# Optimization experiments

Measured on AMD Instinct MI355X. Metric: run time of the kernel, lower is better.

Reference implementation:

```python
import jax, jax.numpy as jnp
import numpy as np

B, S, HID = 2, 2048, 2048
H, HKV = 16, 4
D = HID // H          # 128
N_REP = H // HKV      # 4
ROPE_THETA = 1000000.0


def _rope_tables(seq_len, head_dim, theta):
    inv_freq = 1.0 / (theta ** (jnp.arange(0, head_dim, 2, dtype=jnp.float32) / head_dim))
    freqs = jnp.arange(seq_len, dtype=jnp.float32)[:, None] * inv_freq[None, :]  # [S, D/2]
    emb = jnp.concatenate([freqs, freqs], axis=-1)  # [S, D]
    return jnp.cos(emb), jnp.sin(emb)


def setup_inputs() -> dict:
    key = jax.random.key(0)
    ks = jax.random.split(key, 6)
    cos, sin = _rope_tables(S, D, ROPE_THETA)
    sc = 0.02
    return {
        "x": jax.random.normal(ks[0], (B, S, HID), jnp.float32),
        "cos": cos,
        "sin": sin,
        "Wq": jax.random.normal(ks[1], (HID, H * D), jnp.float32) * sc,
        "Wk": jax.random.normal(ks[2], (HID, HKV * D), jnp.float32) * sc,
        "Wv": jax.random.normal(ks[3], (HID, HKV * D), jnp.float32) * sc,
        "Wo": jax.random.normal(ks[4], (H * D, HID), jnp.float32) * sc,
    }


def _rotate_half(t):
    t1, t2 = jnp.split(t, 2, axis=-1)
    return jnp.concatenate([-t2, t1], axis=-1)


def reference(x, cos, sin, Wq, Wk, Wv, Wo):
    b, s, _ = x.shape
    q = (x @ Wq).reshape(b, s, H, D)    # [b,s,H,d]
    k = (x @ Wk).reshape(b, s, HKV, D)  # [b,s,Hkv,d]
    v = (x @ Wv).reshape(b, s, HKV, D)

    # RoPE (cos/sin broadcast over head axis)
    c = cos[:s, None, :]  # [s,1,d]
    sn = sin[:s, None, :]
    q = q * c + _rotate_half(q) * sn
    k = k * c + _rotate_half(k) * sn

    # GQA: repeat kv heads (interleaved, matching repeat_kv)
    k = jnp.repeat(k, N_REP, axis=2)  # [b,s,H,d]
    v = jnp.repeat(v, N_REP, axis=2)

    q = q.transpose(0, 2, 1, 3)  # [b,H,s,d]
    k = k.transpose(0, 2, 1, 3)
    v = v.transpose(0, 2, 1, 3)

    scale = 1.0 / jnp.sqrt(jnp.asarray(D, x.dtype))
    scores = jnp.einsum("bhqd,bhkd->bhqk", q, k) * scale
    causal = jnp.tril(jnp.ones((s, s), dtype=bool))
    scores = jnp.where(causal[None, None], scores, jnp.asarray(-jnp.inf, scores.dtype))
    probs = jax.nn.softmax(scores, axis=-1)
    out = jnp.einsum("bhqk,bhkd->bhqd", probs, v)
    out = out.transpose(0, 2, 1, 3).reshape(b, s, H * D)
    return out @ Wo
```

## Files before the change

### kernel.cpp

```cpp
#include <hip/hip_runtime.h>
#include <cstdint>

#define B_    2
#define S_    2048
#define HID_  2048
#define H_    16
#define HKV_  4
#define D_    128
#define SCALE_ 0.08838834764831845f
#define LOG2E_ 1.4426950408889634f
#define K1_   (SCALE_ * LOG2E_)
#define THRS_ 62.75f

typedef __bf16 bf16x8 __attribute__((ext_vector_type(8)));
typedef float  f32x4  __attribute__((ext_vector_type(4)));
using u16 = unsigned short;

static __device__ __forceinline__ u16 f2bf(float f) {
  union { float f; uint32_t u; } c; c.f = f;
  uint32_t u = c.u;
  return (u16)((u + 0x7FFFu + ((u >> 16) & 1u)) >> 16);
}
static __device__ __forceinline__ float bf2f(u16 h) {
  union { uint32_t u; float f; } c; c.u = ((uint32_t)h) << 16;
  return c.f;
}
static __device__ __forceinline__ void async16(const u16* g, u16* lds) {
  __builtin_amdgcn_global_load_lds((const __attribute__((address_space(1))) void*)g,
                                   (__attribute__((address_space(3))) void*)lds, 16, 0, 0);
}

__global__ __launch_bounds__(256) void prep_cast_weights(const float* __restrict__ x,
                                                         const float* __restrict__ Wq,
                                                         const float* __restrict__ Wk,
                                                         const float* __restrict__ Wv,
                                                         const float* __restrict__ Wo,
                                                         u16* __restrict__ xb,
                                                         u16* __restrict__ Wt,
                                                         u16* __restrict__ Wot) {
  __shared__ float tile[32][33];
  const int t = blockIdx.x;
  const int tid = threadIdx.x;
  if (t < 8192) {
    const int i = t * 256 + tid;
    float4 v = ((const float4*)x)[i];
    ushort4 o;
    o.x = f2bf(v.x); o.y = f2bf(v.y); o.z = f2bf(v.z); o.w = f2bf(v.w);
    ((ushort4*)xb)[i] = o;
    return;
  }
  const int tw = t - 8192;
  const float* W; u16* Dst; int N, lt;
  if (tw < 4096)      { W = Wq; Dst = Wt;                        N = 2048; lt = tw; }
  else if (tw < 5120) { W = Wk; Dst = Wt + (size_t)2048 * 2048;  N = 512;  lt = tw - 4096; }
  else if (tw < 6144) { W = Wv; Dst = Wt + (size_t)2560 * 2048;  N = 512;  lt = tw - 5120; }
  else                { W = Wo; Dst = Wot;                       N = 2048; lt = tw - 6144; }
  const int tx = tid & 31, ty = tid >> 5;
  const int tn = N >> 5;
  const int n0 = (lt % tn) * 32, k0 = (lt / tn) * 32;
#pragma unroll
  for (int j = 0; j < 32; j += 8)
    tile[ty + j][tx] = W[(size_t)(k0 + ty + j) * N + n0 + tx];
  __syncthreads();
#pragma unroll
  for (int j = 0; j < 32; j += 8)
    Dst[(size_t)(n0 + ty + j) * 2048 + k0 + tx] = f2bf(tile[tx][ty + j]);
}

__global__ __launch_bounds__(256) void prep_rope_vt(const u16* __restrict__ qkv,
                                                    const float* __restrict__ cosb,
                                                    const float* __restrict__ sinb,
                                                    u16* __restrict__ Qr, u16* __restrict__ Kr,
                                                    u16* __restrict__ Vt) {
  __shared__ u16 tile[32][34];
  const int NQ2 = B_ * S_ * H_ * 32;
  const int NK2 = B_ * S_ * HKV_ * 32;
  const int blk = blockIdx.x;
  const int tid = threadIdx.x;
  if (blk < 10240) {
    const int idx = blk * 256 + tid;
    if (idx < NQ2) {
      const int j = (idx & 31) * 2, rest = idx >> 5;
      const int h = rest & 15, srow = rest >> 4;
      const int s = srow & (S_ - 1);
      const u16* base = qkv + (size_t)srow * 3072 + h * 128;
      const float2 cc = *(const float2*)&cosb[s * 128 + j];
      const float2 ss = *(const float2*)&sinb[s * 128 + j];
      const ushort2 av = *(const ushort2*)&base[j];
      const ushort2 bv = *(const ushort2*)&base[j + 64];
      const float a0 = bf2f(av.x), a1 = bf2f(av.y);
      const float b0 = bf2f(bv.x), b1 = bf2f(bv.y);
      const size_t qo = (((size_t)(srow >> 11) * H_ + h) * S_ + s) * D_;
      ushort2 lo, hi;
      lo.x = f2bf(a0 * cc.x - b0 * ss.x); lo.y = f2bf(a1 * cc.y - b1 * ss.y);
      hi.x = f2bf(b0 * cc.x + a0 * ss.x); hi.y = f2bf(b1 * cc.y + a1 * ss.y);
      *(ushort2*)&Qr[qo + j]      = lo;
      *(ushort2*)&Qr[qo + j + 64] = hi;
    } else if (idx < NQ2 + NK2) {
      const int t2 = idx - NQ2;
      const int j = (t2 & 31) * 2, rest = t2 >> 5;
      const int kv = rest & 3, srow = rest >> 2;
      const int s = srow & (S_ - 1);
      const u16* base = qkv + (size_t)srow * 3072 + 2048 + kv * 128;
      const float2 cc = *(const float2*)&cosb[s * 128 + j];
      const float2 ss = *(const float2*)&sinb[s * 128 + j];
      const ushort2 av = *(const ushort2*)&base[j];
      const ushort2 bv = *(const ushort2*)&base[j + 64];
      const float a0 = bf2f(av.x), a1 = bf2f(av.y);
      const float b0 = bf2f(bv.x), b1 = bf2f(bv.y);
      const size_t ko = (((size_t)(srow >> 11) * HKV_ + kv) * S_ + s) * D_;
      ushort2 lo, hi;
      lo.x = f2bf(a0 * cc.x - b0 * ss.x); lo.y = f2bf(a1 * cc.y - b1 * ss.y);
      hi.x = f2bf(b0 * cc.x + a0 * ss.x); hi.y = f2bf(b1 * cc.y + a1 * ss.y);
      *(ushort2*)&Kr[ko + j]      = lo;
      *(ushort2*)&Kr[ko + j + 64] = hi;
    }
    return;
  }
  const int lt = blk - 10240;
  const int bx = lt & 3, by = (lt >> 2) & 63, mat = lt >> 8;
  const int b = mat >> 2, kv = mat & 3;
  const int d0 = bx * 32, s0 = by * 32;
  const int tx = tid & 31, ty = tid >> 5;
#pragma unroll
  for (int j = 0; j < 32; j += 8)
    tile[ty + j][tx] = qkv[(size_t)(b * S_ + s0 + ty + j) * 3072 + 2560 + kv * 128 + d0 + tx];
  __syncthreads();
  const int sc  = s0 + tx;
  const int t64 = sc & 63;
  const int p   = ((t64 >> 5) * 4 + ((t64 >> 2) & 3)) * 8 + ((t64 >> 4) & 1) * 4 + (t64 & 3);
  const int scp = (sc & ~63) | p;
#pragma unroll
  for (int j = 0; j < 32; j += 8)
    Vt[((size_t)mat * D_ + d0 + ty + j) * S_ + scp] = tile[tx][ty + j];
}

template<int BF16OUT>
__global__ __launch_bounds__(256, 3) void gemm_bt(const u16* __restrict__ A,
                                                  const u16* __restrict__ Bt,
                                                  void* __restrict__ Cv,
                                                  int M, int N, int K, int gx) {
  const int nwg = (int)gridDim.x;
  const int bid = (int)blockIdx.x;
  const int qq = nwg >> 3, rr = nwg & 7;
  const int xcd = bid & 7, pos = bid >> 3;
  const int wg = ((xcd < rr) ? xcd * (qq + 1) : rr * (qq + 1) + (xcd - rr) * qq) + pos;
  const int bm = (wg % gx) * 128;
  const int bn = (wg / gx) * 128;

  __shared__ __align__(16) u16 Ash[128 * 64];
  __shared__ __align__(16) u16 Bsh[128 * 64];
  const int tid = threadIdx.x;
  const int w = tid >> 6, l = tid & 63;
  const int wm = (w >> 1) * 64, wn = (w & 1) * 64;

  const f32x4 z4 = {0.f, 0.f, 0.f, 0.f};
  f32x4 acc[4][4];
#pragma unroll
  for (int i = 0; i < 4; ++i)
#pragma unroll
    for (int j = 0; j < 4; ++j) acc[i][j] = z4;

  const int srow = w * 8 + (l >> 3);
  const int schunk = l & 7;

  for (int k0 = 0; k0 < K; k0 += 64) {
#pragma unroll
    for (int i = 0; i < 4; ++i) {
      const int row = i * 32 + srow;
      const int ch = schunk ^ (row & 7);
      async16(A + (size_t)(bm + row) * K + k0 + ch * 8, &Ash[(i * 4 + w) * 512]);
      async16(Bt + (size_t)(bn + row) * K + k0 + ch * 8, &Bsh[(i * 4 + w) * 512]);
    }
    asm volatile("s_waitcnt vmcnt(0)" ::: "memory");
    __syncthreads();
#pragma unroll
    for (int kc = 0; kc < 2; ++kc) {
      bf16x8 af[4], bfr[4];
#pragma unroll
      for (int mi = 0; mi < 4; ++mi) {
        const int r = wm + mi * 16 + (l & 15);
        const int c2 = (kc * 4 + (l >> 4)) ^ (r & 7);
        af[mi] = *(const bf16x8*)&Ash[r * 64 + c2 * 8];
      }
#pragma unroll
      for (int ni = 0; ni < 4; ++ni) {
        const int r = wn + ni * 16 + (l & 15);
        const int c2 = (kc * 4 + (l >> 4)) ^ (r & 7);
        bfr[ni] = *(const bf16x8*)&Bsh[r * 64 + c2 * 8];
      }
#pragma unroll
      for (int mi = 0; mi < 4; ++mi)
#pragma unroll
        for (int ni = 0; ni < 4; ++ni)
          acc[mi][ni] = __builtin_amdgcn_mfma_f32_16x16x32_bf16(af[mi], bfr[ni], acc[mi][ni], 0, 0, 0);
    }
    __syncthreads();
  }
#pragma unroll
  for (int mi = 0; mi < 4; ++mi) {
    const int r0 = bm + wm + mi * 16 + ((l >> 4) << 2);
#pragma unroll
    for (int ni = 0; ni < 4; ++ni) {
      const int c = bn + wn + ni * 16 + (l & 15);
#pragma unroll
      for (int j = 0; j < 4; ++j) {
        if (BF16OUT) ((u16*)Cv)[(size_t)(r0 + j) * N + c] = f2bf(acc[mi][ni][j]);
        else         ((float*)Cv)[(size_t)(r0 + j) * N + c] = acc[mi][ni][j];
      }
    }
  }
}

__global__ __launch_bounds__(256, 3) void attn_kernel(const u16* __restrict__ Q,
                                                      const u16* __restrict__ Kc,
                                                      const u16* __restrict__ Vt,
                                                      u16* __restrict__ O) {
  const int bid = blockIdx.x;
  const int p   = bid & 7;
  const int hs  = (bid >> 3) & 3;
  const int idx = bid >> 5;
  const int grp = idx >> 3, jj2 = idx & 7;
  const int qt  = (grp == 0) ? (31 - jj2) : (grp == 1) ? jj2
                : (grp == 2) ? (23 - jj2) : (8 + jj2);
  const int b   = p >> 2;
  const int kvh = p & 3;
  const int h   = kvh * 4 + hs;
  const int bh  = b * 16 + h;
  const int tid = threadIdx.x;
  const int w = tid >> 6, l = tid & 63;
  const int g = l >> 4, c = l & 15;
  const int q0 = qt * 64;

  __shared__ __align__(16) u16 Ksh[64 * 128];
  __shared__ __align__(16) u16 VshF[2 * 128 * 64];

  const u16* Kbase = Kc + ((size_t)(b * HKV_ + kvh) * S_) * D_;
  const u16* Vbase = Vt + ((size_t)(b * HKV_ + kvh) * D_) * S_;

  bf16x8 qf[4];
  {
    const u16* qp = Q + ((size_t)bh * S_ + q0 + w * 16 + c) * D_ + g * 8;
#pragma unroll
    for (int kc = 0; kc < 4; ++kc) qf[kc] = *(const bf16x8*)(qp + kc * 32);
  }

  int srcK[4], srcV[4];
#pragma unroll
  for (int i = 0; i < 4; ++i) {
    const int rK = i * 16 + w * 4 + g;
    srcK[i] = rK * 128 + (c ^ (rK & 7)) * 8;
    const int dV = i * 32 + w * 8 + (l >> 3);
    srcV[i] = dV * S_ + ((l & 7) ^ (dV & 7)) * 8;
  }

  const f32x4 z4 = {0.f, 0.f, 0.f, 0.f};
  f32x4 oacc[8];
#pragma unroll
  for (int nb = 0; nb < 8; ++nb) oacc[nb] = z4;
  float m_i = -1e30f, l_i = 0.f;

  auto stageK = [&](int kv0) {
#pragma unroll
    for (int i = 0; i < 4; ++i)
      async16(Kbase + (size_t)kv0 * 128 + srcK[i], &Ksh[i * 2048 + w * 512]);
  };
  auto stageV = [&](int buf, int kv0) {
#pragma unroll
    for (int i = 0; i < 4; ++i)
      async16(Vbase + kv0 + srcV[i], &VshF[buf * 8192 + i * 2048 + w * 512]);
  };

  const int nt = qt + 1;
  stageV(0, 0);
  stageK(0);

  for (int t = 0; t < nt; ++t) {
    const int cur = t & 1;
    asm volatile("s_waitcnt vmcnt(0)" ::: "memory");
    __syncthreads();
    if (t + 1 < nt) stageV(cur ^ 1, (t + 1) << 6);

    f32x4 sf[4];
#pragma unroll
    for (int nb = 0; nb < 4; ++nb) sf[nb] = z4;

    __builtin_amdgcn_s_setprio(1);
#pragma unroll
    for (int kc = 0; kc < 4; ++kc) {
#pragma unroll
      for (int nb = 0; nb < 4; ++nb) {
        const int r = nb * 16 + c;
        const int s2 = (kc * 4 + g) ^ (c & 7);
        const bf16x8 kf = *(const bf16x8*)&Ksh[r * 128 + s2 * 8];
        sf[nb] = __builtin_amdgcn_mfma_f32_16x16x32_bf16(kf, qf[kc], sf[nb], 0, 0, 0);
      }
    }
    __builtin_amdgcn_s_setprio(0);

    __syncthreads();
    if (t + 1 < nt) stageK((t + 1) << 6);

    {
      const int kv0 = t << 6;
      const int qcol = q0 + w * 16 + c;
      const bool doMask = (t == nt - 1);
      float mx = -3e38f;
#pragma unroll
      for (int nb = 0; nb < 4; ++nb)
#pragma unroll
        for (int jj = 0; jj < 4; ++jj) {
          float sv = sf[nb][jj];
          if (doMask) {
            const int kk = kv0 + nb * 16 + g * 4 + jj;
            sv = (kk > qcol) ? -3e38f : sv;
            sf[nb][jj] = sv;
          }
          mx = fmaxf(mx, sv);
        }
      mx = fmaxf(mx, __shfl_xor(mx, 16));
      mx = fmaxf(mx, __shfl_xor(mx, 32));

      if (__all(mx <= m_i + THRS_)) {
        const float mk = m_i * K1_;
        float rs = 0.f;
#pragma unroll
        for (int nb = 0; nb < 4; ++nb)
#pragma unroll
          for (int jj = 0; jj < 4; ++jj) {
            const float p2 = exp2f(fmaf(sf[nb][jj], K1_, -mk));
            sf[nb][jj] = p2;
            rs += p2;
          }
        rs += __shfl_xor(rs, 16);
        rs += __shfl_xor(rs, 32);
        l_i += rs;
      } else {
        const float mnew = fmaxf(m_i, mx);
        const float fsc = exp2f((m_i - mnew) * K1_);
        m_i = mnew;
        const float mk = mnew * K1_;
        float rs = 0.f;
#pragma unroll
        for (int nb = 0; nb < 4; ++nb)
#pragma unroll
          for (int jj = 0; jj < 4; ++jj) {
            const float p2 = exp2f(fmaf(sf[nb][jj], K1_, -mk));
            sf[nb][jj] = p2;
            rs += p2;
          }
        rs += __shfl_xor(rs, 16);
        rs += __shfl_xor(rs, 32);
        l_i = l_i * fsc + rs;
        float fq[4];
#pragma unroll
        for (int j = 0; j < 4; ++j) fq[j] = __shfl(fsc, g * 4 + j);
#pragma unroll
        for (int nb = 0; nb < 8; ++nb)
#pragma unroll
          for (int j = 0; j < 4; ++j) oacc[nb][j] *= fq[j];
      }
    }

    bf16x8 pa, pb;
#pragma unroll
    for (int jj = 0; jj < 4; ++jj) {
      pa[jj] = (__bf16)sf[0][jj]; pa[4 + jj] = (__bf16)sf[1][jj];
      pb[jj] = (__bf16)sf[2][jj]; pb[4 + jj] = (__bf16)sf[3][jj];
    }

    const char* Vb = (const char*)&VshF[cur * 8192] + c * 128;
    __builtin_amdgcn_s_setprio(1);
#pragma unroll
    for (int kc2 = 0; kc2 < 2; ++kc2) {
      const bf16x8 pfr = kc2 ? pb : pa;
      const int s2v = ((kc2 * 4 + g) ^ (c & 7)) << 4;
#pragma unroll
      for (int nb = 0; nb < 8; ++nb) {
        const bf16x8 vf = *(const bf16x8*)(Vb + nb * 2048 + s2v);
        oacc[nb] = __builtin_amdgcn_mfma_f32_16x16x32_bf16(pfr, vf, oacc[nb], 0, 0, 0);
      }
    }
    __builtin_amdgcn_s_setprio(0);
  }

#pragma unroll
  for (int j = 0; j < 4; ++j) {
    const float li = __shfl(l_i, g * 4 + j);
    const float inv = 1.f / li;
    const int srow = q0 + w * 16 + g * 4 + j;
    u16* op = O + ((size_t)(b * S_ + srow)) * HID_ + h * D_ + c;
#pragma unroll
    for (int nb = 0; nb < 8; ++nb) op[nb * 16] = f2bf(oacc[nb][j] * inv);
  }
}

extern "C" void kernel_launch(void* const* d_in, const int* in_sizes, int n_in,
                              void* d_out, int out_size, void* d_ws, size_t ws_size,
                              hipStream_t stream) {
  const float* x    = (const float*)d_in[0];
  const float* cosb = (const float*)d_in[1];
  const float* sinb = (const float*)d_in[2];
  const float* Wq   = (const float*)d_in[3];
  const float* Wk   = (const float*)d_in[4];
  const float* Wv   = (const float*)d_in[5];
  const float* Wo   = (const float*)d_in[6];
  float* out = (float*)d_out;

  u16*   xb   = (u16*)d_ws;
  u16*   Wt   = xb  + (size_t)4096 * 2048;
  u16*   Wot  = Wt  + (size_t)3072 * 2048;
  u16*   qkv  = Wot + (size_t)2048 * 2048;
  u16*   Qr   = qkv + (size_t)4096 * 3072;
  u16*   Kr   = Qr  + (size_t)B_ * H_ * S_ * D_;
  u16*   Vtb  = Kr  + (size_t)B_ * HKV_ * S_ * D_;
  u16*   Ob   = Vtb + (size_t)B_ * HKV_ * S_ * D_;

  prep_cast_weights<<<dim3(18432), 256, 0, stream>>>(x, Wq, Wk, Wv, Wo, xb, Wt, Wot);

  gemm_bt<1><<<dim3(768), 256, 0, stream>>>(xb, Wt, qkv, 4096, 3072, 2048, 32);

  prep_rope_vt<<<dim3(12288), 256, 0, stream>>>(qkv, cosb, sinb, Qr, Kr, Vtb);

  attn_kernel<<<dim3(1024), 256, 0, stream>>>(Qr, Kr, Vtb, Ob);

  gemm_bt<0><<<dim3(512), 256, 0, stream>>>(Ob, Wot, out, 4096, 2048, 2048, 32);
}
```

Baseline: 199.0 us.

## Fuse Q RoPE into attention and V transpose into QKV GEMM epilogue

Removes the separate rope/transpose pass for Q and V. The QKV GEMM epilogue now writes the V columns straight into the permuted transposed Vt layout, and attention loads raw Q from the qkv buffer and applies RoPE in registers. A small kernel still rotates K. This avoids writing and re-reading the Q buffer and the V staging traffic, at the cost of extra cos/sin loads and ALU work in the attention prologue and strided ushort4 stores in the GEMM epilogue.

```diff
diff --git a/kernel.cpp b/kernel.cpp
--- a/kernel.cpp
+++ b/kernel.cpp
@@ -67,78 +67,34 @@
     Dst[(size_t)(n0 + ty + j) * 2048 + k0 + tx] = f2bf(tile[tx][ty + j]);
 }
 
-__global__ __launch_bounds__(256) void prep_rope_vt(const u16* __restrict__ qkv,
-                                                    const float* __restrict__ cosb,
-                                                    const float* __restrict__ sinb,
-                                                    u16* __restrict__ Qr, u16* __restrict__ Kr,
-                                                    u16* __restrict__ Vt) {
-  __shared__ u16 tile[32][34];
-  const int NQ2 = B_ * S_ * H_ * 32;
-  const int NK2 = B_ * S_ * HKV_ * 32;
-  const int blk = blockIdx.x;
-  const int tid = threadIdx.x;
-  if (blk < 10240) {
-    const int idx = blk * 256 + tid;
-    if (idx < NQ2) {
-      const int j = (idx & 31) * 2, rest = idx >> 5;
-      const int h = rest & 15, srow = rest >> 4;
-      const int s = srow & (S_ - 1);
-      const u16* base = qkv + (size_t)srow * 3072 + h * 128;
-      const float2 cc = *(const float2*)&cosb[s * 128 + j];
-      const float2 ss = *(const float2*)&sinb[s * 128 + j];
-      const ushort2 av = *(const ushort2*)&base[j];
-      const ushort2 bv = *(const ushort2*)&base[j + 64];
-      const float a0 = bf2f(av.x), a1 = bf2f(av.y);
-      const float b0 = bf2f(bv.x), b1 = bf2f(bv.y);
-      const size_t qo = (((size_t)(srow >> 11) * H_ + h) * S_ + s) * D_;
-      ushort2 lo, hi;
-      lo.x = f2bf(a0 * cc.x - b0 * ss.x); lo.y = f2bf(a1 * cc.y - b1 * ss.y);
-      hi.x = f2bf(b0 * cc.x + a0 * ss.x); hi.y = f2bf(b1 * cc.y + a1 * ss.y);
-      *(ushort2*)&Qr[qo + j]      = lo;
-      *(ushort2*)&Qr[qo + j + 64] = hi;
-    } else if (idx < NQ2 + NK2) {
-      const int t2 = idx - NQ2;
-      const int j = (t2 & 31) * 2, rest = t2 >> 5;
-      const int kv = rest & 3, srow = rest >> 2;
-      const int s = srow & (S_ - 1);
-      const u16* base = qkv + (size_t)srow * 3072 + 2048 + kv * 128;
-      const float2 cc = *(const float2*)&cosb[s * 128 + j];
-      const float2 ss = *(const float2*)&sinb[s * 128 + j];
-      const ushort2 av = *(const ushort2*)&base[j];
-      const ushort2 bv = *(const ushort2*)&base[j + 64];
-      const float a0 = bf2f(av.x), a1 = bf2f(av.y);
-      const float b0 = bf2f(bv.x), b1 = bf2f(bv.y);
-      const size_t ko = (((size_t)(srow >> 11) * HKV_ + kv) * S_ + s) * D_;
-      ushort2 lo, hi;
-      lo.x = f2bf(a0 * cc.x - b0 * ss.x); lo.y = f2bf(a1 * cc.y - b1 * ss.y);
-      hi.x = f2bf(b0 * cc.x + a0 * ss.x); hi.y = f2bf(b1 * cc.y + a1 * ss.y);
-      *(ushort2*)&Kr[ko + j]      = lo;
-      *(ushort2*)&Kr[ko + j + 64] = hi;
-    }
-    return;
-  }
-  const int lt = blk - 10240;
-  const int bx = lt & 3, by = (lt >> 2) & 63, mat = lt >> 8;
-  const int b = mat >> 2, kv = mat & 3;
-  const int d0 = bx * 32, s0 = by * 32;
-  const int tx = tid & 31, ty = tid >> 5;
-#pragma unroll
-  for (int j = 0; j < 32; j += 8)
-    tile[ty + j][tx] = qkv[(size_t)(b * S_ + s0 + ty + j) * 3072 + 2560 + kv * 128 + d0 + tx];
-  __syncthreads();
-  const int sc  = s0 + tx;
-  const int t64 = sc & 63;
-  const int p   = ((t64 >> 5) * 4 + ((t64 >> 2) & 3)) * 8 + ((t64 >> 4) & 1) * 4 + (t64 & 3);
-  const int scp = (sc & ~63) | p;
-#pragma unroll
-  for (int j = 0; j < 32; j += 8)
-    Vt[((size_t)mat * D_ + d0 + ty + j) * S_ + scp] = tile[tx][ty + j];
-}
-
-template<int BF16OUT>
+__global__ __launch_bounds__(256) void prep_rope_k(const u16* __restrict__ qkv,
+                                                   const float* __restrict__ cosb,
+                                                   const float* __restrict__ sinb,
+                                                   u16* __restrict__ Kr) {
+  const int idx = blockIdx.x * 256 + threadIdx.x;
+  const int j = (idx & 31) * 2, rest = idx >> 5;
+  const int kv = rest & 3, srow = rest >> 2;
+  const int s = srow & (S_ - 1);
+  const u16* base = qkv + (size_t)srow * 3072 + 2048 + kv * 128;
+  const float2 cc = *(const float2*)&cosb[s * 128 + j];
+  const float2 ss = *(const float2*)&sinb[s * 128 + j];
+  const ushort2 av = *(const ushort2*)&base[j];
+  const ushort2 bv = *(const ushort2*)&base[j + 64];
+  const float a0 = bf2f(av.x), a1 = bf2f(av.y);
+  const float b0 = bf2f(bv.x), b1 = bf2f(bv.y);
+  const size_t ko = (((size_t)(srow >> 11) * HKV_ + kv) * S_ + s) * D_;
+  ushort2 lo, hi;
+  lo.x = f2bf(a0 * cc.x - b0 * ss.x); lo.y = f2bf(a1 * cc.y - b1 * ss.y);
+  hi.x = f2bf(b0 * cc.x + a0 * ss.x); hi.y = f2bf(b1 * cc.y + a1 * ss.y);
+  *(ushort2*)&Kr[ko + j]      = lo;
+  *(ushort2*)&Kr[ko + j + 64] = hi;
+}
+
+template<int MODE>
 __global__ __launch_bounds__(256, 3) void gemm_bt(const u16* __restrict__ A,
                                                   const u16* __restrict__ Bt,
                                                   void* __restrict__ Cv,
+                                                  u16* __restrict__ Vt,
                                                   int M, int N, int K, int gx) {
   const int nwg = (int)gridDim.x;
   const int bid = (int)blockIdx.x;
@@ -197,22 +153,47 @@
     }
     __syncthreads();
   }
-#pragma unroll
-  for (int mi = 0; mi < 4; ++mi) {
-    const int r0 = bm + wm + mi * 16 + ((l >> 4) << 2);
-#pragma unroll
-    for (int ni = 0; ni < 4; ++ni) {
-      const int c = bn + wn + ni * 16 + (l & 15);
-#pragma unroll
-      for (int j = 0; j < 4; ++j) {
-        if (BF16OUT) ((u16*)Cv)[(size_t)(r0 + j) * N + c] = f2bf(acc[mi][ni][j]);
-        else         ((float*)Cv)[(size_t)(r0 + j) * N + c] = acc[mi][ni][j];
-      }
-    }
-  }
-}
-
-__global__ __launch_bounds__(256, 3) void attn_kernel(const u16* __restrict__ Q,
+
+  if (MODE == 1 && bn >= 2560) {
+    const int kv = (bn - 2560) >> 7;
+#pragma unroll
+    for (int mi = 0; mi < 4; ++mi) {
+      const int r0 = bm + wm + mi * 16 + ((l >> 4) << 2);
+      const int bb = r0 >> 11;
+      const int s0 = r0 & (S_ - 1);
+      const int a  = (s0 & 63) >> 2;
+      const int pb = ((a >> 3) * 4 + (a & 3)) * 8 + ((a >> 2) & 1) * 4;
+      const int spb = (s0 & ~63) | pb;
+      u16* vb = Vt + ((size_t)(bb * HKV_ + kv) * D_) * S_ + spb;
+#pragma unroll
+      for (int ni = 0; ni < 4; ++ni) {
+        const int d = wn + ni * 16 + (l & 15);
+        ushort4 o;
+        o.x = f2bf(acc[mi][ni][0]); o.y = f2bf(acc[mi][ni][1]);
+        o.z = f2bf(acc[mi][ni][2]); o.w = f2bf(acc[mi][ni][3]);
+        *(ushort4*)&vb[(size_t)d * S_] = o;
+      }
+    }
+  } else {
+#pragma unroll
+    for (int mi = 0; mi < 4; ++mi) {
+      const int r0 = bm + wm + mi * 16 + ((l >> 4) << 2);
+#pragma unroll
+      for (int ni = 0; ni < 4; ++ni) {
+        const int c = bn + wn + ni * 16 + (l & 15);
+#pragma unroll
+        for (int j = 0; j < 4; ++j) {
+          if (MODE == 1) ((u16*)Cv)[(size_t)(r0 + j) * N + c] = f2bf(acc[mi][ni][j]);
+          else           ((float*)Cv)[(size_t)(r0 + j) * N + c] = acc[mi][ni][j];
+        }
+      }
+    }
+  }
+}
+
+__global__ __launch_bounds__(256, 3) void attn_kernel(const u16* __restrict__ qkv,
+                                                      const float* __restrict__ cosb,
+                                                      const float* __restrict__ sinb,
                                                       const u16* __restrict__ Kc,
                                                       const u16* __restrict__ Vt,
                                                       u16* __restrict__ O) {
@@ -226,7 +207,6 @@
   const int b   = p >> 2;
   const int kvh = p & 3;
   const int h   = kvh * 4 + hs;
-  const int bh  = b * 16 + h;
   const int tid = threadIdx.x;
   const int w = tid >> 6, l = tid & 63;
   const int g = l >> 4, c = l & 15;
@@ -240,9 +220,30 @@
 
   bf16x8 qf[4];
   {
-    const u16* qp = Q + ((size_t)bh * S_ + q0 + w * 16 + c) * D_ + g * 8;
-#pragma unroll
-    for (int kc = 0; kc < 4; ++kc) qf[kc] = *(const bf16x8*)(qp + kc * 32);
+    const int s_q = q0 + w * 16 + c;
+    const u16* qp = qkv + (size_t)(b * S_ + s_q) * 3072 + h * 128 + g * 8;
+    bf16x8 qraw[4];
+#pragma unroll
+    for (int kc = 0; kc < 4; ++kc) qraw[kc] = *(const bf16x8*)(qp + kc * 32);
+    const float* cp = cosb + s_q * 128 + g * 8;
+    const float* sp = sinb + s_q * 128 + g * 8;
+#pragma unroll
+    for (int kcp = 0; kcp < 2; ++kcp) {
+      float cl[8], sl[8];
+      *(float4*)&cl[0] = *(const float4*)(cp + kcp * 32);
+      *(float4*)&cl[4] = *(const float4*)(cp + kcp * 32 + 4);
+      *(float4*)&sl[0] = *(const float4*)(sp + kcp * 32);
+      *(float4*)&sl[4] = *(const float4*)(sp + kcp * 32 + 4);
+      bf16x8 lo, hi;
+#pragma unroll
+      for (int j = 0; j < 8; ++j) {
+        const float a  = (float)qraw[kcp][j];
+        const float b2 = (float)qraw[kcp + 2][j];
+        lo[j] = (__bf16)(a * cl[j] - b2 * sl[j]);
+        hi[j] = (__bf16)(b2 * cl[j] + a * sl[j]);
+      }
+      qf[kcp] = lo; qf[kcp + 2] = hi;
+    }
   }
 
   int srcK[4], srcV[4];
@@ -411,18 +412,17 @@
   u16*   Wt   = xb  + (size_t)4096 * 2048;
   u16*   Wot  = Wt  + (size_t)3072 * 2048;
   u16*   qkv  = Wot + (size_t)2048 * 2048;
-  u16*   Qr   = qkv + (size_t)4096 * 3072;
-  u16*   Kr   = Qr  + (size_t)B_ * H_ * S_ * D_;
+  u16*   Kr   = qkv + (size_t)4096 * 3072;
   u16*   Vtb  = Kr  + (size_t)B_ * HKV_ * S_ * D_;
   u16*   Ob   = Vtb + (size_t)B_ * HKV_ * S_ * D_;
 
   prep_cast_weights<<<dim3(18432), 256, 0, stream>>>(x, Wq, Wk, Wv, Wo, xb, Wt, Wot);
 
-  gemm_bt<1><<<dim3(768), 256, 0, stream>>>(xb, Wt, qkv, 4096, 3072, 2048, 32);
-
-  prep_rope_vt<<<dim3(12288), 256, 0, stream>>>(qkv, cosb, sinb, Qr, Kr, Vtb);
-
-  attn_kernel<<<dim3(1024), 256, 0, stream>>>(Qr, Kr, Vtb, Ob);
-
-  gemm_bt<0><<<dim3(512), 256, 0, stream>>>(Ob, Wot, out, 4096, 2048, 2048, 32);
-}
+  gemm_bt<1><<<dim3(768), 256, 0, stream>>>(xb, Wt, qkv, Vtb, 4096, 3072, 2048, 32);
+
+  prep_rope_k<<<dim3(2048), 256, 0, stream>>>(qkv, cosb, sinb, Kr);
+
+  attn_kernel<<<dim3(1024), 256, 0, stream>>>(qkv, cosb, sinb, Kr, Vtb, Ob);
+
+  gemm_bt<0><<<dim3(512), 256, 0, stream>>>(Ob, Wot, out, nullptr, 4096, 2048, 2048, 32);
+}
```

After: 195.9 us, median of 2. No clear change (-1.6%).
